# Kernel optimization log

Measured on AMD Instinct MI355X. Metric: run time of the kernel, lower is better.

The kernel has to match this reference:

```python
import jax, jax.numpy as jnp
import numpy as np

INPUT_DIM = 22
HIDDEN_DIM = 9
TAGSET_SIZE = 4
SEQ_LEN = 524288


def setup_inputs() -> dict:
    key = jax.random.key(0)
    ks = jax.random.split(key, 7)
    s = 1.0 / np.sqrt(HIDDEN_DIM)  # PyTorch LSTM/Linear default init scale
    x = jax.random.normal(ks[0], (SEQ_LEN, INPUT_DIM), dtype=jnp.float32)
    w_ih = jax.random.uniform(ks[1], (4 * HIDDEN_DIM, INPUT_DIM), jnp.float32, -s, s)
    w_hh = jax.random.uniform(ks[2], (4 * HIDDEN_DIM, HIDDEN_DIM), jnp.float32, -s, s)
    b_ih = jax.random.uniform(ks[3], (4 * HIDDEN_DIM,), jnp.float32, -s, s)
    b_hh = jax.random.uniform(ks[4], (4 * HIDDEN_DIM,), jnp.float32, -s, s)
    w_out = jax.random.uniform(ks[5], (TAGSET_SIZE, HIDDEN_DIM), jnp.float32, -s, s)
    b_out = jax.random.uniform(ks[6], (TAGSET_SIZE,), jnp.float32, -s, s)
    return {"input_sequence": x, "w_ih": w_ih, "w_hh": w_hh, "b_ih": b_ih,
            "b_hh": b_hh, "w_out": w_out, "b_out": b_out}


def reference(input_sequence, w_ih, w_hh, b_ih, b_hh, w_out, b_out):
    H = w_hh.shape[1]
    # Precompute input contribution to gates for all timesteps: [S, 4H]
    x_gates = input_sequence @ w_ih.T + (b_ih + b_hh)

    def step(carry, xg):
        h, c = carry
        gates = xg + h @ w_hh.T  # [4H], PyTorch gate order: i, f, g, o
        i = jax.nn.sigmoid(gates[0 * H:1 * H])
        f = jax.nn.sigmoid(gates[1 * H:2 * H])
        g = jnp.tanh(gates[2 * H:3 * H])
        o = jax.nn.sigmoid(gates[3 * H:4 * H])
        c_new = f * c + i * g
        h_new = o * jnp.tanh(c_new)
        return (h_new, c_new), h_new

    h0 = jnp.zeros((H,), dtype=input_sequence.dtype)
    c0 = jnp.zeros((H,), dtype=input_sequence.dtype)
    _, hs = jax.lax.scan(step, (h0, c0), x_gates)  # hs: [S, H]

    tag_space = hs @ w_out.T + b_out  # [S, tagset_size]
    return jax.nn.log_softmax(tag_space, axis=1)
```

## Files before the change

kernel.cpp:

```cpp
#include <hip/hip_runtime.h>
#include <hip/hip_fp16.h>

#define S_LEN   524288
#define IN_D    22
#define HID     9
#define NTAG    4
#define CHUNK   128
#define BURN    64
#define NCHUNK  (S_LEN / CHUNK)
#define WPB     4
#define PF      8
#define GT      8

#define XGP_HALFS ((size_t)S_LEN * 36)
#define H_HALFS   ((size_t)S_LEN * HID)
#define WS_NEED   ((XGP_HALFS + H_HALFS) * 2)

template <int PAT>
__device__ __forceinline__ float qperm(float v) {
  return __int_as_float(__builtin_amdgcn_update_dpp(
      0, __float_as_int(v), PAT, 0xF, 0xF, true));
}

__global__ __launch_bounds__(256)
void xg_gemm(const float* __restrict__ x, const float* __restrict__ w_ih,
             const float* __restrict__ b_ih, const float* __restrict__ b_hh,
             __half* __restrict__ xgp)
{
  const int tid = (int)blockIdx.x * 256 + threadIdx.x;
  const int t8  = tid / 36;
  const int l   = tid - t8 * 36;
  const int u = l >> 2, g = l & 3, row = g * HID + u;
  const float mex = (g == 2) ? -2.885390082f : -1.442695041f;

  float wr[IN_D];
#pragma unroll
  for (int k = 0; k < IN_D; ++k) wr[k] = w_ih[row * IN_D + k] * mex;
  const float bb = (b_ih[row] + b_hh[row]) * mex;

  const long tb = (long)t8 * GT;
#pragma unroll
  for (int j = 0; j < GT; ++j) {
    const float* xr = x + (tb + j) * IN_D;
    float xv[IN_D];
#pragma unroll
    for (int c = 0; c < IN_D / 2; ++c)
      *(float2*)(&xv[2 * c]) = *(const float2*)(xr + 2 * c);
    float a0 = bb, a1 = 0.f;
#pragma unroll
    for (int k = 0; k < IN_D; ++k) {
      if (k & 1) a1 = fmaf(xv[k], wr[k], a1);
      else       a0 = fmaf(xv[k], wr[k], a0);
    }
    xgp[(tb + j) * 36 + l] = __float2half(a0 + a1);
  }
}

__global__ __launch_bounds__(256, 4)
void lstm_scan2(const __half* __restrict__ xgp,
                const float* __restrict__ w_hh,
                __half* __restrict__ hout)
{
  const int tid  = threadIdx.x;
  const int wv   = tid >> 6;
  const int lane = tid & 63;
  const int u = lane >> 2, g = lane & 3;
  const bool act = (u < HID);
  const int row  = act ? (g * HID + u) : 0;
  const long ll  = (lane < 36) ? lane : 35;
  const float mexp = (g == 2) ? -2.885390082f : -1.442695041f;
  const float smul = (g == 2) ? 2.f : 1.f;
  const float soff = (g == 2) ? -1.f : 0.f;

  float whh[HID];
#pragma unroll
  for (int k = 0; k < HID; ++k)
    whh[k] = (act ? w_hh[row * HID + k] : 0.f) * mexp;

  const int chunk = (int)blockIdx.x * WPB + wv;
  const int start = chunk * CHUNK;
  const int t0    = (start >= BURN) ? (start - BURN) : 0;
  const int nstep = start + CHUNK - t0;

  __half xq[PF];
#pragma unroll
  for (int j = 0; j < PF; ++j) xq[j] = xgp[(long)(t0 + j) * 36 + ll];

  float sh[HID];
#pragma unroll
  for (int k = 0; k < HID; ++k) sh[k] = 0.f;
  float cst = 0.f;

  for (int b = 0; b < nstep / PF; ++b) {
    const int tb = t0 + b * PF;
    const bool outp = (tb >= start);
#pragma unroll
    for (int j = 0; j < PF; ++j) {
      float a0 = __half2float(xq[j]);
      {
        long tt = tb + j + PF; if (tt >= S_LEN) tt = S_LEN - 1;
        xq[j] = xgp[tt * 36 + ll];
      }
      float a1 = 0.f;
#pragma unroll
      for (int k = 0; k < HID; ++k) {
        if (k & 1) a1 = fmaf(sh[k], whh[k], a1);
        else       a0 = fmaf(sh[k], whh[k], a0);
      }
      const float pre = a0 + a1;
      const float ex  = __builtin_amdgcn_exp2f(pre);
      const float gv  = fmaf(__builtin_amdgcn_rcpf(1.f + ex), smul, soff);

      const float fg = qperm<0x39>(gv);
      const float gg = qperm<0x4E>(gv);
      const float og = qperm<0x93>(gv);
      cst = fmaf(fg, cst, gv * gg);
      const float e2 = __builtin_amdgcn_exp2f(cst * -2.885390082f);
      const float th = fmaf(__builtin_amdgcn_rcpf(1.f + e2), 2.f, -1.f);
      const float hv = og * th;

#pragma unroll
      for (int k = 0; k < HID; ++k)
        sh[k] = __int_as_float(
            __builtin_amdgcn_readlane(__float_as_int(hv), 4 * k));

      if (outp && g == 0 && u < HID)
        hout[(long)(tb + j) * HID + u] = __float2half(hv);
    }
  }
}

__global__ __launch_bounds__(256)
void head_k(const __half* __restrict__ h, const float* __restrict__ w_out,
            const float* __restrict__ b_out, float* __restrict__ out)
{
  const int tid = (int)blockIdx.x * 256 + threadIdx.x;
  const int t = tid >> 2, tag = tid & 3;
  float wo[HID];
#pragma unroll
  for (int k = 0; k < HID; ++k) wo[k] = w_out[tag * HID + k];
  float acc = b_out[tag];
  const __half* hr = h + (long)t * HID;
#pragma unroll
  for (int k = 0; k < HID; ++k) acc = fmaf(__half2float(hr[k]), wo[k], acc);

  float m = fmaxf(acc, qperm<0xB1>(acc));
  m = fmaxf(m, qperm<0x4E>(m));
  const float xm = acc - m;
  const float ee = __builtin_amdgcn_exp2f(xm * 1.442695041f);
  float sm = ee + qperm<0xB1>(ee);
  sm = sm + qperm<0x4E>(sm);
  out[tid] = fmaf(-0.69314718056f, __builtin_amdgcn_logf(sm), xm);
}

#define TILE    16
#define ROWF    24
#define TILEF   (TILE * ROWF)
#define NLOADS  (TILEF / 64)

__global__ __launch_bounds__(256, 4)
void lstm_chunk_scan(const float* __restrict__ x,
                     const float* __restrict__ w_ih,
                     const float* __restrict__ w_hh,
                     const float* __restrict__ b_ih,
                     const float* __restrict__ b_hh,
                     const float* __restrict__ w_out,
                     const float* __restrict__ b_out,
                     float* __restrict__ out)
{
  __shared__ __align__(16) float lds[WPB * 2 * TILEF];

  const int tid  = threadIdx.x;
  const int wv   = __builtin_amdgcn_readfirstlane(tid >> 6);
  const int lane = tid & 63;
  const int u    = lane >> 2;
  const int g    = lane & 3;
  const bool act = (u < HID);
  const int row  = act ? (g * HID + u) : 0;

  float wih[IN_D], whh[HID], wo[HID];
#pragma unroll
  for (int k = 0; k < IN_D; ++k) wih[k] = act ? w_ih[row * IN_D + k] : 0.f;
#pragma unroll
  for (int k = 0; k < HID; ++k)  whh[k] = act ? w_hh[row * HID + k] : 0.f;
  const float bias = act ? (b_ih[row] + b_hh[row]) : 0.f;
  const int orow = (lane < NTAG) ? lane : 0;
  float wo_b = b_out[orow];
#pragma unroll
  for (int k = 0; k < HID; ++k)  wo[k] = w_out[orow * HID + k];
  if (lane >= NTAG) { wo_b = 0.f; }

  const float mexp = (g == 2) ? -2.885390082f : -1.442695041f;
  const float smul = (g == 2) ? 2.f : 1.f;
  const float soff = (g == 2) ? -1.f : 0.f;

  const int chunk = __builtin_amdgcn_readfirstlane((int)blockIdx.x * WPB + wv);
  const int start = chunk * CHUNK;
  const int t0    = (start >= BURN) ? (start - BURN) : 0;
  const int nstep = start + CHUNK - t0;
  const int ntile = nstep / TILE;

  float* myl = lds + wv * 2 * TILEF;

  int goff[NLOADS];
#pragma unroll
  for (int cc = 0; cc < NLOADS; ++cc) {
    int slot = cc * 64 + lane;
    int r = slot / ROWF;
    int col = slot - r * ROWF;
    if (col >= IN_D) col = IN_D - 1;
    goff[cc] = r * IN_D + col;
  }
  const long XMAX = (long)S_LEN * IN_D - 1;

  float stage[NLOADS];
  {
    long tb = (long)t0 * IN_D;
#pragma unroll
    for (int cc = 0; cc < NLOADS; ++cc) {
      long gi = tb + goff[cc];
      if (gi > XMAX) gi = XMAX;
      stage[cc] = x[gi];
    }
#pragma unroll
    for (int cc = 0; cc < NLOADS; ++cc) myl[cc * 64 + lane] = stage[cc];
  }

  float sh[HID];
#pragma unroll
  for (int k = 0; k < HID; ++k) sh[k] = 0.f;
  float cst = 0.f;

  for (int ti = 0; ti < ntile; ++ti) {
    {
      long tb = (long)(t0 + (ti + 1) * TILE) * IN_D;
#pragma unroll
      for (int cc = 0; cc < NLOADS; ++cc) {
        long gi = tb + goff[cc];
        if (gi > XMAX) gi = XMAX;
        stage[cc] = x[gi];
      }
    }

    const float* rb = myl + (ti & 1) * TILEF;
    const int tbase = t0 + ti * TILE;
    const bool outp = (tbase >= start);

#pragma unroll
    for (int s = 0; s < TILE; ++s) {
      const float* xr = rb + s * ROWF;
      float xv[22];
      *(float4*)(&xv[0])  = *(const float4*)(xr + 0);
      *(float4*)(&xv[4])  = *(const float4*)(xr + 4);
      *(float4*)(&xv[8])  = *(const float4*)(xr + 8);
      *(float4*)(&xv[12]) = *(const float4*)(xr + 12);
      *(float4*)(&xv[16]) = *(const float4*)(xr + 16);
      *(float2*)(&xv[20]) = *(const float2*)(xr + 20);

      float a0 = bias, a1 = 0.f;
#pragma unroll
      for (int k = 0; k < IN_D; ++k) {
        if (k & 1) a1 = fmaf(xv[k], wih[k], a1);
        else       a0 = fmaf(xv[k], wih[k], a0);
      }
#pragma unroll
      for (int k = 0; k < HID; ++k) {
        if (k & 1) a1 = fmaf(sh[k], whh[k], a1);
        else       a0 = fmaf(sh[k], whh[k], a0);
      }
      float pre = a0 + a1;

      float ex = __builtin_amdgcn_exp2f(pre * mexp);
      float gv = fmaf(__builtin_amdgcn_rcpf(1.f + ex), smul, soff);

      float fg = qperm<0x39>(gv);
      float gg = qperm<0x4E>(gv);
      float og = qperm<0x93>(gv);
      cst = fmaf(fg, cst, gv * gg);
      float e2 = __builtin_amdgcn_exp2f(cst * -2.885390082f);
      float th = fmaf(__builtin_amdgcn_rcpf(1.f + e2), 2.f, -1.f);
      float hv = og * th;

#pragma unroll
      for (int k = 0; k < HID; ++k)
        sh[k] = __int_as_float(
            __builtin_amdgcn_readlane(__float_as_int(hv), 4 * k));

      if (outp) {
        float acc = wo_b;
#pragma unroll
        for (int k = 0; k < HID; ++k) acc = fmaf(sh[k], wo[k], acc);
        float m = fmaxf(acc, qperm<0xB1>(acc));
        m = fmaxf(m, qperm<0x4E>(m));
        float xm = acc - m;
        float ee = __builtin_amdgcn_exp2f(xm * 1.442695041f);
        float sm = ee + qperm<0xB1>(ee);
        sm = sm + qperm<0x4E>(sm);
        float res = fmaf(-0.69314718056f, __builtin_amdgcn_logf(sm), xm);
        if (lane < NTAG) out[(long)(tbase + s) * NTAG + lane] = res;
      }
    }

    float* wb = myl + ((ti + 1) & 1) * TILEF;
#pragma unroll
    for (int cc = 0; cc < NLOADS; ++cc) wb[cc * 64 + lane] = stage[cc];
  }
}

extern "C" void kernel_launch(void* const* d_in, const int* in_sizes, int n_in,
                              void* d_out, int out_size, void* d_ws, size_t ws_size,
                              hipStream_t stream) {
  (void)in_sizes; (void)n_in; (void)out_size;
  const float* x     = (const float*)d_in[0];
  const float* w_ih  = (const float*)d_in[1];
  const float* w_hh  = (const float*)d_in[2];
  const float* b_ih  = (const float*)d_in[3];
  const float* b_hh  = (const float*)d_in[4];
  const float* w_out = (const float*)d_in[5];
  const float* b_out = (const float*)d_in[6];
  float* out = (float*)d_out;

  if (ws_size >= WS_NEED) {
    __half* xgp = (__half*)d_ws;
    __half* h   = (__half*)d_ws + XGP_HALFS;
    hipLaunchKernelGGL(xg_gemm, dim3(36 * (S_LEN / GT) / 256), dim3(256), 0,
                       stream, x, w_ih, b_ih, b_hh, xgp);
    hipLaunchKernelGGL(lstm_scan2, dim3(NCHUNK / WPB), dim3(256), 0, stream,
                       xgp, w_hh, h);
    hipLaunchKernelGGL(head_k, dim3(S_LEN * NTAG / 256), dim3(256), 0, stream,
                       h, w_out, b_out, out);
  } else {
    hipLaunchKernelGGL(lstm_chunk_scan, dim3(NCHUNK / WPB), dim3(256), 0,
                       stream, x, w_ih, w_hh, b_ih, b_hh, w_out, b_out, out);
  }
}
```

Measured before the change: 215.4 us.

## Restructure input-gate GEMM to one timestep per thread, shrink burn-in to 48

The input-projection kernel now gives each thread a whole timestep: it loads the 22 inputs once and computes all 36 gate preactivations, reading scaled weights from shared memory as float4s and writing packed half pairs with vector stores. Before, each thread owned one gate row and reloaded the input row for every gate, which repeated x reads 36 times. The LSTM warmup (burn-in) before each chunk is also cut from 64 to 48 steps, which shortens the serial scan. The shorter warmup may weaken hidden-state convergence and so affect accuracy, and the per-thread stores are strided by 72 bytes, which may coalesce less well.

```diff
diff --git a/kernel.cpp b/kernel.cpp
--- a/kernel.cpp
+++ b/kernel.cpp
@@ -6,11 +6,10 @@
 #define HID     9
 #define NTAG    4
 #define CHUNK   128
-#define BURN    64
+#define BURN    48
 #define NCHUNK  (S_LEN / CHUNK)
 #define WPB     4
 #define PF      8
-#define GT      8
 
 #define XGP_HALFS ((size_t)S_LEN * 36)
 #define H_HALFS   ((size_t)S_LEN * HID)
@@ -27,33 +26,57 @@
              const float* __restrict__ b_ih, const float* __restrict__ b_hh,
              __half* __restrict__ xgp)
 {
-  const int tid = (int)blockIdx.x * 256 + threadIdx.x;
-  const int t8  = tid / 36;
-  const int l   = tid - t8 * 36;
-  const int u = l >> 2, g = l & 3, row = g * HID + u;
-  const float mex = (g == 2) ? -2.885390082f : -1.442695041f;
-
-  float wr[IN_D];
-#pragma unroll
-  for (int k = 0; k < IN_D; ++k) wr[k] = w_ih[row * IN_D + k] * mex;
-  const float bb = (b_ih[row] + b_hh[row]) * mex;
-
-  const long tb = (long)t8 * GT;
-#pragma unroll
-  for (int j = 0; j < GT; ++j) {
-    const float* xr = x + (tb + j) * IN_D;
-    float xv[IN_D];
-#pragma unroll
-    for (int c = 0; c < IN_D / 2; ++c)
-      *(float2*)(&xv[2 * c]) = *(const float2*)(xr + 2 * c);
-    float a0 = bb, a1 = 0.f;
-#pragma unroll
-    for (int k = 0; k < IN_D; ++k) {
-      if (k & 1) a1 = fmaf(xv[k], wr[k], a1);
-      else       a0 = fmaf(xv[k], wr[k], a0);
-    }
-    xgp[(tb + j) * 36 + l] = __float2half(a0 + a1);
-  }
+  __shared__ __align__(16) float wl[36][24];
+  const int tid = threadIdx.x;
+  for (int i = tid; i < 36 * 24; i += 256) {
+    const int l = i / 24, c = i - l * 24;
+    const int g = l & 3, u = l >> 2;
+    const int row = g * HID + u;
+    const float mex = (g == 2) ? -2.885390082f : -1.442695041f;
+    float v = 0.f;
+    if (c < IN_D)       v = w_ih[row * IN_D + c] * mex;
+    else if (c == IN_D) v = (b_ih[row] + b_hh[row]) * mex;
+    wl[l][c] = v;
+  }
+  __syncthreads();
+
+  const long t = (long)blockIdx.x * 256 + tid;
+  const float* xr = x + t * IN_D;
+  float xv[IN_D];
+#pragma unroll
+  for (int c = 0; c < IN_D / 2; ++c)
+    *(float2*)(&xv[2 * c]) = *(const float2*)(xr + 2 * c);
+
+  unsigned int pk[18];
+#pragma unroll
+  for (int l2 = 0; l2 < 18; ++l2) {
+    float r[2];
+#pragma unroll
+    for (int s = 0; s < 2; ++s) {
+      const int l = 2 * l2 + s;
+      const float4* w4 = (const float4*)&wl[l][0];
+      const float4 w0 = w4[0], w1 = w4[1], w2 = w4[2];
+      const float4 w3 = w4[3], w4v = w4[4], w5 = w4[5];
+      float a0 = w5.z, a1 = 0.f;
+      a0 = fmaf(xv[0],  w0.x, a0); a1 = fmaf(xv[1],  w0.y, a1);
+      a0 = fmaf(xv[2],  w0.z, a0); a1 = fmaf(xv[3],  w0.w, a1);
+      a0 = fmaf(xv[4],  w1.x, a0); a1 = fmaf(xv[5],  w1.y, a1);
+      a0 = fmaf(xv[6],  w1.z, a0); a1 = fmaf(xv[7],  w1.w, a1);
+      a0 = fmaf(xv[8],  w2.x, a0); a1 = fmaf(xv[9],  w2.y, a1);
+      a0 = fmaf(xv[10], w2.z, a0); a1 = fmaf(xv[11], w2.w, a1);
+      a0 = fmaf(xv[12], w3.x, a0); a1 = fmaf(xv[13], w3.y, a1);
+      a0 = fmaf(xv[14], w3.z, a0); a1 = fmaf(xv[15], w3.w, a1);
+      a0 = fmaf(xv[16], w4v.x, a0); a1 = fmaf(xv[17], w4v.y, a1);
+      a0 = fmaf(xv[18], w4v.z, a0); a1 = fmaf(xv[19], w4v.w, a1);
+      a0 = fmaf(xv[20], w5.x, a0); a1 = fmaf(xv[21], w5.y, a1);
+      r[s] = a0 + a1;
+    }
+    __half2 h2; h2.x = __float2half(r[0]); h2.y = __float2half(r[1]);
+    pk[l2] = *(unsigned int*)&h2;
+  }
+  uint2* po = (uint2*)(xgp + t * 36);
+#pragma unroll
+  for (int i = 0; i < 9; ++i) po[i] = make_uint2(pk[2 * i], pk[2 * i + 1]);
 }
 
 __global__ __launch_bounds__(256, 4)
@@ -68,9 +91,9 @@
   const bool act = (u < HID);
   const int row  = act ? (g * HID + u) : 0;
   const long ll  = (lane < 36) ? lane : 35;
-  const float mexp = (g == 2) ? -2.885390082f : -1.442695041f;
   const float smul = (g == 2) ? 2.f : 1.f;
   const float soff = (g == 2) ? -1.f : 0.f;
+  const float mexp = (g == 2) ? -2.885390082f : -1.442695041f;
 
   float whh[HID];
 #pragma unroll
@@ -323,8 +346,8 @@
   if (ws_size >= WS_NEED) {
     __half* xgp = (__half*)d_ws;
     __half* h   = (__half*)d_ws + XGP_HALFS;
-    hipLaunchKernelGGL(xg_gemm, dim3(36 * (S_LEN / GT) / 256), dim3(256), 0,
-                       stream, x, w_ih, b_ih, b_hh, xgp);
+    hipLaunchKernelGGL(xg_gemm, dim3(S_LEN / 256), dim3(256), 0, stream,
+                       x, w_ih, b_ih, b_hh, xgp);
     hipLaunchKernelGGL(lstm_scan2, dim3(NCHUNK / WPB), dim3(256), 0, stream,
                        xgp, w_hh, h);
     hipLaunchKernelGGL(head_k, dim3(S_LEN * NTAG / 256), dim3(256), 0, stream,
```

After: 181.3 us. 1.19x faster.

## Interleave two LSTM chunks per wave, pad gate buffer, use packed-half input GEMM

Applied to the files above, without the earlier changes.

The scan kernel now runs two independent chunks per wavefront, interleaving their recurrence steps to hide the latency of the serial dependency chain. The warm-up length drops from 64 to 48. The gate buffer gets low padding filled by a memset, so the first chunk needs no boundary clamping. The input projection is rewritten with packed half2 FMAs, LDS-staged weights and DPP broadcasts of x. These trade register pressure and half-precision accumulation error for more throughput, and the shorter warm-up plus the 0x7B pad fill may reduce accuracy.

```diff
diff --git a/kernel.cpp b/kernel.cpp
--- a/kernel.cpp
+++ b/kernel.cpp
@@ -6,13 +6,15 @@
 #define HID     9
 #define NTAG    4
 #define CHUNK   128
-#define BURN    64
+#define BURN    48
 #define NCHUNK  (S_LEN / CHUNK)
 #define WPB     4
 #define PF      8
-#define GT      8
-
-#define XGP_HALFS ((size_t)S_LEN * 36)
+
+#define PAD_LO  48
+#define PAD_HI  8
+#define XGP_ROWS ((size_t)PAD_LO + S_LEN + PAD_HI)
+#define XGP_HALFS (XGP_ROWS * 36)
 #define H_HALFS   ((size_t)S_LEN * HID)
 #define WS_NEED   ((XGP_HALFS + H_HALFS) * 2)
 
@@ -21,43 +23,98 @@
   return __int_as_float(__builtin_amdgcn_update_dpp(
       0, __float_as_int(v), PAT, 0xF, 0xF, true));
 }
-
-__global__ __launch_bounds__(256)
-void xg_gemm(const float* __restrict__ x, const float* __restrict__ w_ih,
-             const float* __restrict__ b_ih, const float* __restrict__ b_hh,
-             __half* __restrict__ xgp)
+template <int PAT>
+__device__ __forceinline__ unsigned qpu(unsigned v) {
+  return (unsigned)__builtin_amdgcn_update_dpp(
+      0, (int)v, PAT, 0xF, 0xF, true);
+}
+__device__ __forceinline__ unsigned h2u(__half2 h) { return __builtin_bit_cast(unsigned, h); }
+__device__ __forceinline__ __half2 u2h(unsigned u) { return __builtin_bit_cast(__half2, u); }
+
+#define GBLK 1024
+#define GNP  16
+__global__ __launch_bounds__(256, 1)
+void xg_gemm3(const float* __restrict__ x, const float* __restrict__ w_ih,
+              const float* __restrict__ b_ih, const float* __restrict__ b_hh,
+              __half* __restrict__ xgp)
 {
-  const int tid = (int)blockIdx.x * 256 + threadIdx.x;
-  const int t8  = tid / 36;
-  const int l   = tid - t8 * 36;
-  const int u = l >> 2, g = l & 3, row = g * HID + u;
-  const float mex = (g == 2) ? -2.885390082f : -1.442695041f;
-
-  float wr[IN_D];
-#pragma unroll
-  for (int k = 0; k < IN_D; ++k) wr[k] = w_ih[row * IN_D + k] * mex;
-  const float bb = (b_ih[row] + b_hh[row]) * mex;
-
-  const long tb = (long)t8 * GT;
-#pragma unroll
-  for (int j = 0; j < GT; ++j) {
-    const float* xr = x + (tb + j) * IN_D;
-    float xv[IN_D];
-#pragma unroll
-    for (int c = 0; c < IN_D / 2; ++c)
-      *(float2*)(&xv[2 * c]) = *(const float2*)(xr + 2 * c);
-    float a0 = bb, a1 = 0.f;
+  __shared__ float wl[36][23];
+  const int tid = threadIdx.x;
+  for (int i = tid; i < 36 * 23; i += 256) {
+    const int r = i / 23, c = i - r * 23;
+    wl[r][c] = (c < IN_D) ? w_ih[r * IN_D + c] : (b_ih[r] + b_hh[r]);
+  }
+  __syncthreads();
+
+  const int lane = tid & 63;
+  const int wv   = tid >> 6;
+  const int g    = lane & 3;
+  const int qd   = lane >> 2;
+
+  __half2 wpk[5][IN_D], bpk[5];
+#pragma unroll
+  for (int p = 0; p < 5; ++p) {
+    const int r0 = g * HID + 2 * p;
+    const bool h1 = (2 * p + 1 < HID);
+    const int r1 = h1 ? (r0 + 1) : r0;
+#pragma unroll
+    for (int k = 0; k < IN_D; ++k)
+      wpk[p][k] = __floats2half2_rn(wl[r0][k], h1 ? wl[r1][k] : 0.f);
+    bpk[p] = __floats2half2_rn(wl[r0][IN_D], h1 ? wl[r1][IN_D] : 0.f);
+  }
+  const float mexg = (g == 2) ? -2.885390082f : -1.442695041f;
+  const __half2 mex2 = __float2half2_rn(mexg);
+  const int b0 = (g < 3) ? g * 6 : 16;
+
+  const long tbase = (long)blockIdx.x * GBLK + wv * 16 + qd;
+#pragma unroll 1
+  for (int ps = 0; ps < GNP; ++ps) {
+    const long t = tbase + (long)ps * 64;
+    const float* xr = x + t * IN_D + b0;
+    float2 L0 = *(const float2*)(xr);
+    float2 L1 = *(const float2*)(xr + 2);
+    float2 L2 = *(const float2*)(xr + 4);
+    unsigned sx[6];
+    sx[0] = h2u(__float2half2_rn(L0.x)); sx[1] = h2u(__float2half2_rn(L0.y));
+    sx[2] = h2u(__float2half2_rn(L1.x)); sx[3] = h2u(__float2half2_rn(L1.y));
+    sx[4] = h2u(__float2half2_rn(L2.x)); sx[5] = h2u(__float2half2_rn(L2.y));
+
+    unsigned xs[IN_D];
+    xs[0]  = qpu<0x00>(sx[0]); xs[1]  = qpu<0x00>(sx[1]);
+    xs[2]  = qpu<0x00>(sx[2]); xs[3]  = qpu<0x00>(sx[3]);
+    xs[4]  = qpu<0x00>(sx[4]); xs[5]  = qpu<0x00>(sx[5]);
+    xs[6]  = qpu<0x55>(sx[0]); xs[7]  = qpu<0x55>(sx[1]);
+    xs[8]  = qpu<0x55>(sx[2]); xs[9]  = qpu<0x55>(sx[3]);
+    xs[10] = qpu<0x55>(sx[4]); xs[11] = qpu<0x55>(sx[5]);
+    xs[12] = qpu<0xAA>(sx[0]); xs[13] = qpu<0xAA>(sx[1]);
+    xs[14] = qpu<0xAA>(sx[2]); xs[15] = qpu<0xAA>(sx[3]);
+    xs[16] = qpu<0xAA>(sx[4]); xs[17] = qpu<0xAA>(sx[5]);
+    xs[18] = qpu<0xFF>(sx[2]); xs[19] = qpu<0xFF>(sx[3]);
+    xs[20] = qpu<0xFF>(sx[4]); xs[21] = qpu<0xFF>(sx[5]);
+
+    __half2 acc[5];
+#pragma unroll
+    for (int p = 0; p < 5; ++p) acc[p] = bpk[p];
 #pragma unroll
     for (int k = 0; k < IN_D; ++k) {
-      if (k & 1) a1 = fmaf(xv[k], wr[k], a1);
-      else       a0 = fmaf(xv[k], wr[k], a0);
+      const __half2 xk = u2h(xs[k]);
+#pragma unroll
+      for (int p = 0; p < 5; ++p) acc[p] = __hfma2(wpk[p][k], xk, acc[p]);
     }
-    xgp[(tb + j) * 36 + l] = __float2half(a0 + a1);
+#pragma unroll
+    for (int p = 0; p < 5; ++p) acc[p] = __hmul2(acc[p], mex2);
+
+    __half* po = xgp + t * 36 + g * HID;
+    po[0] = __low2half(acc[0]); po[1] = __high2half(acc[0]);
+    po[2] = __low2half(acc[1]); po[3] = __high2half(acc[1]);
+    po[4] = __low2half(acc[2]); po[5] = __high2half(acc[2]);
+    po[6] = __low2half(acc[3]); po[7] = __high2half(acc[3]);
+    po[8] = __low2half(acc[4]);
   }
 }
 
 __global__ __launch_bounds__(256, 4)
-void lstm_scan2(const __half* __restrict__ xgp,
+void lstm_scan3(const __half* __restrict__ xgp,
                 const float* __restrict__ w_hh,
                 __half* __restrict__ hout)
 {
@@ -67,67 +124,76 @@
   const int u = lane >> 2, g = lane & 3;
   const bool act = (u < HID);
   const int row  = act ? (g * HID + u) : 0;
-  const long ll  = (lane < 36) ? lane : 35;
-  const float mexp = (g == 2) ? -2.885390082f : -1.442695041f;
+  const int ll   = (lane < 36) ? (g * HID + u) : 35;
   const float smul = (g == 2) ? 2.f : 1.f;
   const float soff = (g == 2) ? -1.f : 0.f;
+  const float mexp = (g == 2) ? -2.885390082f : -1.442695041f;
 
   float whh[HID];
 #pragma unroll
   for (int k = 0; k < HID; ++k)
     whh[k] = (act ? w_hh[row * HID + k] : 0.f) * mexp;
 
-  const int chunk = (int)blockIdx.x * WPB + wv;
-  const int start = chunk * CHUNK;
-  const int t0    = (start >= BURN) ? (start - BURN) : 0;
-  const int nstep = start + CHUNK - t0;
-
-  __half xq[PF];
-#pragma unroll
-  for (int j = 0; j < PF; ++j) xq[j] = xgp[(long)(t0 + j) * 36 + ll];
-
-  float sh[HID];
-#pragma unroll
-  for (int k = 0; k < HID; ++k) sh[k] = 0.f;
-  float cst = 0.f;
-
-  for (int b = 0; b < nstep / PF; ++b) {
-    const int tb = t0 + b * PF;
-    const bool outp = (tb >= start);
+  const int gw = (int)blockIdx.x * WPB + wv;
+  const int startA = (2 * gw) * CHUNK;
+  const int startB = startA + CHUNK;
+  const long t0A = (long)startA - BURN;
+  const long t0B = (long)startB - BURN;
+  const __half* gA = xgp + t0A * 36 + ll;
+  const __half* gB = xgp + t0B * 36 + ll;
+
+  __half xqA[PF], xqB[PF];
+#pragma unroll
+  for (int j = 0; j < PF; ++j) { xqA[j] = gA[j * 36]; xqB[j] = gB[j * 36]; }
+
+  float shA[HID], shB[HID];
+#pragma unroll
+  for (int k = 0; k < HID; ++k) { shA[k] = 0.f; shB[k] = 0.f; }
+  float cstA = 0.f, cstB = 0.f;
+
+#define STEP(xq, gptr, sh, cst, hv, S)                                  \
+  {                                                                     \
+    float a0 = __half2float(xq[j]);                                     \
+    xq[j] = gptr[(S + PF) * 36];                                        \
+    float a1 = 0.f;                                                     \
+    _Pragma("unroll")                                                   \
+    for (int k = 0; k < HID; ++k) {                                     \
+      if (k & 1) a1 = fmaf(sh[k], whh[k], a1);                          \
+      else       a0 = fmaf(sh[k], whh[k], a0);                          \
+    }                                                                   \
+    const float pre = a0 + a1;                                          \
+    const float ex  = __builtin_amdgcn_exp2f(pre);                      \
+    const float gv  = fmaf(__builtin_amdgcn_rcpf(1.f + ex), smul, soff);\
+    const float fg = qperm<0x39>(gv);                                   \
+    const float gg = qperm<0x4E>(gv);                                   \
+    const float og = qperm<0x93>(gv);                                   \
+    cst = fmaf(fg, cst, gv * gg);                                       \
+    const float e2 = __builtin_amdgcn_exp2f(cst * -2.885390082f);       \
+    const float th = fmaf(__builtin_amdgcn_rcpf(1.f + e2), 2.f, -1.f);  \
+    hv = og * th;                                                       \
+    _Pragma("unroll")                                                   \
+    for (int k = 0; k < HID; ++k)                                       \
+      sh[k] = __int_as_float(                                           \
+          __builtin_amdgcn_readlane(__float_as_int(hv), 4 * k));        \
+  }
+
+  const int NSTEP = CHUNK + BURN;
+  for (int b = 0; b < NSTEP / PF; ++b) {
+    const int sb = b * PF;
+    const bool outp = sb >= BURN;
 #pragma unroll
     for (int j = 0; j < PF; ++j) {
-      float a0 = __half2float(xq[j]);
-      {
-        long tt = tb + j + PF; if (tt >= S_LEN) tt = S_LEN - 1;
-        xq[j] = xgp[tt * 36 + ll];
+      const int s = sb + j;
+      float hvA, hvB;
+      STEP(xqA, gA, shA, cstA, hvA, s)
+      STEP(xqB, gB, shB, cstB, hvB, s)
+      if (outp && g == 0 && act) {
+        hout[(long)(startA + s - BURN) * HID + u] = __float2half(hvA);
+        hout[(long)(startB + s - BURN) * HID + u] = __float2half(hvB);
       }
-      float a1 = 0.f;
-#pragma unroll
-      for (int k = 0; k < HID; ++k) {
-        if (k & 1) a1 = fmaf(sh[k], whh[k], a1);
-        else       a0 = fmaf(sh[k], whh[k], a0);
-      }
-      const float pre = a0 + a1;
-      const float ex  = __builtin_amdgcn_exp2f(pre);
-      const float gv  = fmaf(__builtin_amdgcn_rcpf(1.f + ex), smul, soff);
-
-      const float fg = qperm<0x39>(gv);
-      const float gg = qperm<0x4E>(gv);
-      const float og = qperm<0x93>(gv);
-      cst = fmaf(fg, cst, gv * gg);
-      const float e2 = __builtin_amdgcn_exp2f(cst * -2.885390082f);
-      const float th = fmaf(__builtin_amdgcn_rcpf(1.f + e2), 2.f, -1.f);
-      const float hv = og * th;
-
-#pragma unroll
-      for (int k = 0; k < HID; ++k)
-        sh[k] = __int_as_float(
-            __builtin_amdgcn_readlane(__float_as_int(hv), 4 * k));
-
-      if (outp && g == 0 && u < HID)
-        hout[(long)(tb + j) * HID + u] = __float2half(hv);
     }
   }
+#undef STEP
 }
 
 __global__ __launch_bounds__(256)
@@ -321,11 +387,13 @@
   float* out = (float*)d_out;
 
   if (ws_size >= WS_NEED) {
-    __half* xgp = (__half*)d_ws;
-    __half* h   = (__half*)d_ws + XGP_HALFS;
-    hipLaunchKernelGGL(xg_gemm, dim3(36 * (S_LEN / GT) / 256), dim3(256), 0,
-                       stream, x, w_ih, b_ih, b_hh, xgp);
-    hipLaunchKernelGGL(lstm_scan2, dim3(NCHUNK / WPB), dim3(256), 0, stream,
+    __half* xgp_base = (__half*)d_ws;
+    __half* xgp = xgp_base + (size_t)PAD_LO * 36;
+    __half* h   = xgp_base + XGP_HALFS;
+    hipMemsetAsync(xgp_base, 0x7B, (size_t)PAD_LO * 36 * 2, stream);
+    hipLaunchKernelGGL(xg_gemm3, dim3(S_LEN / GBLK), dim3(256), 0, stream,
+                       x, w_ih, b_ih, b_hh, xgp);
+    hipLaunchKernelGGL(lstm_scan3, dim3(NCHUNK / 2 / WPB), dim3(256), 0, stream,
                        xgp, w_hh, h);
     hipLaunchKernelGGL(head_k, dim3(S_LEN * NTAG / 256), dim3(256), 0, stream,
                        h, w_out, b_out, out);
```

Result: faster. 175.7 us (-18.4%).
